# Kernel tuning notes

Hardware: AMD Instinct MI355X
Metric: run time of the kernel (lower is better)

The kernel has to match this reference:

```python
import jax, jax.numpy as jnp
import numpy as np

DROPOUT_P = 0.0  # undefined global `dropout_p` in source; pinned to 0 (identity) for determinism


def setup_inputs() -> dict:
    key = jax.random.key(0)
    k1, k2, k3 = jax.random.split(key, 3)
    B, Lq, Lk, D = 16, 4096, 4096, 64
    return {
        "query": jax.random.normal(k1, (B, Lq, D), dtype=jnp.float32),
        "key": jax.random.normal(k2, (B, Lk, D), dtype=jnp.float32),
        "value": jax.random.normal(k3, (B, Lk, D), dtype=jnp.float32),
        "scale_factor": jnp.ones((1,), dtype=jnp.float32),
    }


def reference(query, key, value, scale_factor):
    # scores: [B, Lq, Lk] -- the large HBM-materialized intermediate
    scores = jnp.einsum("bqd,bkd->bqk", query, key) / scale_factor
    probs = jax.nn.softmax(scores, axis=-1)
    # dropout with p = DROPOUT_P = 0.0 is the identity
    out = jnp.einsum("bqk,bkd->bqd", probs, value)
    return out
```

## Files before the change

kernel.cpp:

```cpp
#include <hip/hip_runtime.h>
#include <hip/hip_fp16.h>

typedef _Float16 half2_t __attribute__((ext_vector_type(2)));
typedef _Float16 half4_t __attribute__((ext_vector_type(4)));
typedef _Float16 half8_t __attribute__((ext_vector_type(8)));
typedef float   float4_t __attribute__((ext_vector_type(4)));
typedef float  float16_t __attribute__((ext_vector_type(16)));

static __device__ __forceinline__ half2_t cvt_pk(float a, float b) {
    return __builtin_bit_cast(half2_t, __builtin_amdgcn_cvt_pkrtz(a, b));
}
static __device__ __forceinline__ half4_t cvt_pk4(float a, float b, float c, float d) {
    half2_t lo = cvt_pk(a, b), hi = cvt_pk(c, d);
    half4_t r;
    r[0] = lo[0]; r[1] = lo[1]; r[2] = hi[0]; r[3] = hi[1];
    return r;
}
static __device__ __forceinline__ half8_t cvt_pk8(const float4& a, const float4& b) {
    half4_t lo = cvt_pk4(a.x, a.y, a.z, a.w);
    half4_t hi = cvt_pk4(b.x, b.y, b.z, b.w);
    return __builtin_shufflevector(lo, hi, 0, 1, 2, 3, 4, 5, 6, 7);
}
static __device__ __forceinline__ half8_t join8(half4_t lo, half4_t hi) {
    return __builtin_shufflevector(lo, hi, 0, 1, 2, 3, 4, 5, 6, 7);
}

namespace {
constexpr int kB       = 16;
constexpr int kL       = 4096;
constexpr int kD       = 64;
constexpr int kQTile   = 128;
constexpr int kBK      = 64;
constexpr int kTiles   = kL / kBK;
constexpr int kSplit   = 2;
constexpr int kTilesHf = kTiles / kSplit;
constexpr int kTileH   = kBK * kD;
constexpr int kKStride = 72;
constexpr int kVStride = 72;
constexpr size_t kWsHalves = (size_t)kB * kTiles * kTileH;
constexpr size_t kOHalves  = (size_t)kB * kL * kD;
}


__global__ __launch_bounds__(256) void prep_kv(const float* __restrict__ K,
                                               const float* __restrict__ V,
                                               _Float16* __restrict__ Kws,
                                               _Float16* __restrict__ Vws)
{
    int blk = blockIdx.x;
    const int tid = threadIdx.x;
    if (blk < kB * kTiles) {
        const float* src = K + (size_t)blk * kTileH;
        _Float16* dst = Kws + (size_t)blk * kTileH;
#pragma unroll
        for (int i = 0; i < 2; ++i) {
            const int task = tid + 256 * i;
            const int row  = task >> 3;
            const int g    = task & 7;
            const int srow = (row & ~12) | ((row & 4) << 1) | ((row & 8) >> 1);
            const float* p = src + srow * kD + g * 8;
            const float4 a  = *(const float4*)p;
            const float4 b2 = *(const float4*)(p + 4);
            *(half8_t*)(dst + task * 8) = cvt_pk8(a, b2);
        }
    } else {
        blk -= kB * kTiles;
        const float* src = V + (size_t)blk * kTileH;
        _Float16* dst = Vws + (size_t)blk * kTileH;
        const int d  = tid & 63;
        const int vw = tid >> 6;
#pragma unroll
        for (int i = 0; i < 2; ++i) {
            const int c8 = vw * 2 + i;
            const int k0 = c8 * 8;
            float p[8];
#pragma unroll
            for (int j = 0; j < 8; ++j) p[j] = src[(k0 + j) * kD + d];
            half4_t lo = cvt_pk4(p[0], p[1], p[2], p[3]);
            half4_t hi = cvt_pk4(p[4], p[5], p[6], p[7]);
            *(half8_t*)(dst + (c8 * 64 + d) * 8) = join8(lo, hi);
        }
    }
}

__global__ __launch_bounds__(256, 3)
void fa_fwd(const float* __restrict__ Q, const _Float16* __restrict__ Kws,
            const _Float16* __restrict__ Vws, const float* __restrict__ scale_ptr,
            float* __restrict__ Out, _Float16* __restrict__ O2ws,
            float* __restrict__ Mlws)
{
    __shared__ __align__(16) _Float16 Ksh[kBK * kKStride];
    __shared__ __align__(16) _Float16 Vsh[kD * kVStride];

    const int tid  = threadIdx.x;
    const int wave = tid >> 6;
    const int lane = tid & 63;
    const int l31  = lane & 31;
    const int hi   = lane >> 5;

    const int b  = blockIdx.y;
    const int hf = blockIdx.z;
    const int q0 = blockIdx.x * kQTile + wave * 32;

    const int task0 = tid, task1 = tid + 256;
    const int vd = tid & 63;
    const int vw = tid >> 6;

    const float qscale = 1.4426950408889634f / scale_ptr[0];

    const float*    Qb = Q   + (size_t)b * kL * kD;
    const _Float16* Kt = Kws + ((size_t)b * kTiles + (size_t)hf * kTilesHf) * kTileH;
    const _Float16* Vt = Vws + ((size_t)b * kTiles + (size_t)hf * kTilesHf) * kTileH;

    half8_t qfrag[4];
    {
        const float* qrow = Qb + (size_t)(q0 + l31) * kD;
#pragma unroll
        for (int kd = 0; kd < 4; ++kd) {
            const float* p = qrow + kd * 16 + hi * 8;
            half8_t h;
#pragma unroll
            for (int j = 0; j < 8; ++j) h[j] = (_Float16)(p[j] * qscale);
            qfrag[kd] = h;
        }
    }

    float16_t O[2];
    O[0] = (float16_t)0.0f;
    O[1] = (float16_t)0.0f;
    float m_run = -__builtin_inff();
    float l_run = 0.0f;
    const float16_t Zc = (float16_t)0.0f;

    half8_t kp[2], vp[2];
    kp[0] = *(const half8_t*)(Kt + task0 * 8);
    kp[1] = *(const half8_t*)(Kt + task1 * 8);
    vp[0] = *(const half8_t*)(Vt + ((vw * 2 + 0) * 64 + vd) * 8);
    vp[1] = *(const half8_t*)(Vt + ((vw * 2 + 1) * 64 + vd) * 8);

    for (int t = 0; t < kTilesHf; ++t) {
        __syncthreads();

        *(half8_t*)(&Ksh[(task0 >> 3) * kKStride + (task0 & 7) * 8]) = kp[0];
        *(half8_t*)(&Ksh[(task1 >> 3) * kKStride + (task1 & 7) * 8]) = kp[1];
        *(half8_t*)(&Vsh[vd * kVStride + (vw * 2 + 0) * 8]) = vp[0];
        *(half8_t*)(&Vsh[vd * kVStride + (vw * 2 + 1) * 8]) = vp[1];
        __syncthreads();

        {
            const int nt = (t + 1) & (kTilesHf - 1);
            const _Float16* kn = Kt + (size_t)nt * kTileH;
            const _Float16* vn = Vt + (size_t)nt * kTileH;
            kp[0] = *(const half8_t*)(kn + task0 * 8);
            kp[1] = *(const half8_t*)(kn + task1 * 8);
            vp[0] = *(const half8_t*)(vn + ((vw * 2 + 0) * 64 + vd) * 8);
            vp[1] = *(const half8_t*)(vn + ((vw * 2 + 1) * 64 + vd) * 8);
        }

        float16_t S0, S1;
        {
            half8_t kf0, kf1;
            kf0 = *(const half8_t*)(&Ksh[(l31)      * kKStride + 0 * 16 + hi * 8]);
            kf1 = *(const half8_t*)(&Ksh[(32 + l31) * kKStride + 0 * 16 + hi * 8]);
            S0 = __builtin_amdgcn_mfma_f32_32x32x16_f16(kf0, qfrag[0], Zc, 0, 0, 0);
            S1 = __builtin_amdgcn_mfma_f32_32x32x16_f16(kf1, qfrag[0], Zc, 0, 0, 0);
#pragma unroll
            for (int kd = 1; kd < 4; ++kd) {
                kf0 = *(const half8_t*)(&Ksh[(l31)      * kKStride + kd * 16 + hi * 8]);
                kf1 = *(const half8_t*)(&Ksh[(32 + l31) * kKStride + kd * 16 + hi * 8]);
                S0 = __builtin_amdgcn_mfma_f32_32x32x16_f16(kf0, qfrag[kd], S0, 0, 0, 0);
                S1 = __builtin_amdgcn_mfma_f32_32x32x16_f16(kf1, qfrag[kd], S1, 0, 0, 0);
            }
        }

#define M4(v,a) fmaxf(fmaxf(v[a], v[(a)+1]), fmaxf(v[(a)+2], v[(a)+3]))
        float pm = fmaxf(
            fmaxf(fmaxf(M4(S0, 0), M4(S0, 4)), fmaxf(M4(S0, 8), M4(S0, 12))),
            fmaxf(fmaxf(M4(S1, 0), M4(S1, 4)), fmaxf(M4(S1, 8), M4(S1, 12))));
#undef M4
        pm = fmaxf(pm, __shfl_xor(pm, 32));

        const bool need = pm > m_run + 8.0f;
        if (__ballot(need)) {
            const float mn    = fmaxf(m_run, pm);
            const float alpha = __builtin_amdgcn_exp2f(m_run - mn);
            m_run = mn;
            l_run *= alpha;
#pragma unroll
            for (int r = 0; r < 16; ++r) { O[0][r] *= alpha; O[1][r] *= alpha; }
        }

#pragma unroll
        for (int r = 0; r < 16; ++r) {
            S0[r] = __builtin_amdgcn_exp2f(S0[r] - m_run);
            S1[r] = __builtin_amdgcn_exp2f(S1[r] - m_run);
        }
        half8_t pf[4];
        pf[0] = join8(cvt_pk4(S0[0],  S0[1],  S0[2],  S0[3]),
                      cvt_pk4(S0[4],  S0[5],  S0[6],  S0[7]));
        pf[1] = join8(cvt_pk4(S0[8],  S0[9],  S0[10], S0[11]),
                      cvt_pk4(S0[12], S0[13], S0[14], S0[15]));
        pf[2] = join8(cvt_pk4(S1[0],  S1[1],  S1[2],  S1[3]),
                      cvt_pk4(S1[4],  S1[5],  S1[6],  S1[7]));
        pf[3] = join8(cvt_pk4(S1[8],  S1[9],  S1[10], S1[11]),
                      cvt_pk4(S1[12], S1[13], S1[14], S1[15]));
#define A4(v,a) ((v[a] + v[(a)+1]) + (v[(a)+2] + v[(a)+3]))
        float lt = ((A4(S0, 0) + A4(S0, 4)) + (A4(S0, 8) + A4(S0, 12)))
                 + ((A4(S1, 0) + A4(S1, 4)) + (A4(S1, 8) + A4(S1, 12)));
#undef A4
        lt += __shfl_xor(lt, 32);
        l_run += lt;

#pragma unroll
        for (int kb = 0; kb < 4; ++kb) {
            const half8_t vf0 = *(const half8_t*)(
                &Vsh[(l31)      * kVStride + kb * 16 + hi * 8]);
            const half8_t vf1 = *(const half8_t*)(
                &Vsh[(32 + l31) * kVStride + kb * 16 + hi * 8]);
            O[0] = __builtin_amdgcn_mfma_f32_32x32x16_f16(vf0, pf[kb], O[0], 0, 0, 0);
            O[1] = __builtin_amdgcn_mfma_f32_32x32x16_f16(vf1, pf[kb], O[1], 0, 0, 0);
        }
    }

    const float inv = 1.0f / l_run;
    const int   q   = q0 + l31;
    if (hf == 0) {
        float* op = Out + ((size_t)b * kL + q) * kD;
#pragma unroll
        for (int dt = 0; dt < 2; ++dt)
#pragma unroll
            for (int rr = 0; rr < 4; ++rr) {
                const int d0 = dt * 32 + rr * 8 + hi * 4;
                float4 w;
                w.x = O[dt][rr * 4 + 0] * inv;
                w.y = O[dt][rr * 4 + 1] * inv;
                w.z = O[dt][rr * 4 + 2] * inv;
                w.w = O[dt][rr * 4 + 3] * inv;
                *(float4*)(op + d0) = w;
            }
    } else {
        _Float16* op = O2ws + ((size_t)b * kL + q) * kD;
#pragma unroll
        for (int dt = 0; dt < 2; ++dt)
#pragma unroll
            for (int rr = 0; rr < 4; ++rr) {
                const int d0 = dt * 32 + rr * 8 + hi * 4;
                half4_t w = cvt_pk4(O[dt][rr * 4 + 0] * inv, O[dt][rr * 4 + 1] * inv,
                                    O[dt][rr * 4 + 2] * inv, O[dt][rr * 4 + 3] * inv);
                *(half4_t*)(op + d0) = w;
            }
    }
    if (hi == 0) {
        float* mp = Mlws + (((size_t)b * kL + q) * 2 + hf) * 2;
        mp[0] = m_run;
        mp[1] = l_run;
    }
}

__global__ __launch_bounds__(256)
void combine(float* __restrict__ Out, const _Float16* __restrict__ O2ws,
             const float* __restrict__ Mlws)
{
    const int t   = threadIdx.x;
    const int row = blockIdx.x * 16 + (t >> 4);
    const int d0  = (t & 15) * 4;

    const float m1 = Mlws[(size_t)row * 4 + 0];
    const float l1 = Mlws[(size_t)row * 4 + 1];
    const float m2 = Mlws[(size_t)row * 4 + 2];
    const float l2 = Mlws[(size_t)row * 4 + 3];

    const float m  = fmaxf(m1, m2);
    float w1 = l1 * exp2f(m1 - m);
    float w2 = l2 * exp2f(m2 - m);
    const float inv = 1.0f / (w1 + w2);
    w1 *= inv; w2 *= inv;

    float* op = Out + (size_t)row * kD + d0;
    const _Float16* o2 = O2ws + (size_t)row * kD + d0;
    float4 a = *(const float4*)op;
    const half4_t h = *(const half4_t*)o2;
    a.x = a.x * w1 + (float)h[0] * w2;
    a.y = a.y * w1 + (float)h[1] * w2;
    a.z = a.z * w1 + (float)h[2] * w2;
    a.w = a.w * w1 + (float)h[3] * w2;
    *(float4*)op = a;
}

extern "C" void kernel_launch(void* const* d_in, const int* in_sizes, int n_in,
                              void* d_out, int out_size, void* d_ws, size_t ws_size,
                              hipStream_t stream) {
    const float* Q = (const float*)d_in[0];
    const float* K = (const float*)d_in[1];
    const float* V = (const float*)d_in[2];
    const float* s = (const float*)d_in[3];
    float* out = (float*)d_out;
    _Float16* Kws  = (_Float16*)d_ws;
    _Float16* Vws  = Kws + kWsHalves;
    _Float16* O2ws = Vws + kWsHalves;
    float*    Mlws = (float*)(O2ws + kOHalves);

    prep_kv<<<dim3(2 * kB * kTiles), dim3(256), 0, stream>>>(K, V, Kws, Vws);
    fa_fwd<<<dim3(kL / kQTile, kB, kSplit), dim3(256), 0, stream>>>(Q, Kws, Vws, s, out, O2ws, Mlws);
    combine<<<dim3(kB * kL / 16), dim3(256), 0, stream>>>(out, O2ws, Mlws);
}
```

Baseline: 188.5 us.

## Double-buffer K/V shared tiles, add MFMA priority hints, defer row-sum shuffle

K and V tiles are double-buffered in LDS, so each iteration writes the next tile into the alternate buffer and only one barrier per iteration is needed instead of two. Global prefetch now runs two tiles ahead. The change also raises the occupancy hint to 4 blocks per CU, wraps the MFMA sections in s_setprio, rebuilds the max reduction with 3-input fmax (max3), and moves the cross-half row-sum shuffle out of the loop to the epilogue. The costs are twice the LDS use and a tighter register budget, which may cause spills.

```diff
diff --git a/kernel.cpp b/kernel.cpp
--- a/kernel.cpp
+++ b/kernel.cpp
@@ -23,6 +23,9 @@
 }
 static __device__ __forceinline__ half8_t join8(half4_t lo, half4_t hi) {
     return __builtin_shufflevector(lo, hi, 0, 1, 2, 3, 4, 5, 6, 7);
+}
+static __device__ __forceinline__ float f3(float a, float b, float c) {
+    return fmaxf(fmaxf(a, b), c);
 }
 
 namespace {
@@ -83,14 +86,14 @@
     }
 }
 
-__global__ __launch_bounds__(256, 3)
+__global__ __launch_bounds__(256, 4)
 void fa_fwd(const float* __restrict__ Q, const _Float16* __restrict__ Kws,
             const _Float16* __restrict__ Vws, const float* __restrict__ scale_ptr,
             float* __restrict__ Out, _Float16* __restrict__ O2ws,
             float* __restrict__ Mlws)
 {
-    __shared__ __align__(16) _Float16 Ksh[kBK * kKStride];
-    __shared__ __align__(16) _Float16 Vsh[kD * kVStride];
+    __shared__ __align__(16) _Float16 Ksh[2][kBK * kKStride];
+    __shared__ __align__(16) _Float16 Vsh[2][kD * kVStride];
 
     const int tid  = threadIdx.x;
     const int wave = tid >> 6;
@@ -105,6 +108,10 @@
     const int task0 = tid, task1 = tid + 256;
     const int vd = tid & 63;
     const int vw = tid >> 6;
+    const int koff0 = (task0 >> 3) * kKStride + (task0 & 7) * 8;
+    const int koff1 = (task1 >> 3) * kKStride + (task1 & 7) * 8;
+    const int voff0 = vd * kVStride + (vw * 2 + 0) * 8;
+    const int voff1 = vd * kVStride + (vw * 2 + 1) * 8;
 
     const float qscale = 1.4426950408889634f / scale_ptr[0];
 
@@ -137,18 +144,34 @@
     kp[1] = *(const half8_t*)(Kt + task1 * 8);
     vp[0] = *(const half8_t*)(Vt + ((vw * 2 + 0) * 64 + vd) * 8);
     vp[1] = *(const half8_t*)(Vt + ((vw * 2 + 1) * 64 + vd) * 8);
+    *(half8_t*)(&Ksh[0][koff0]) = kp[0];
+    *(half8_t*)(&Ksh[0][koff1]) = kp[1];
+    *(half8_t*)(&Vsh[0][voff0]) = vp[0];
+    *(half8_t*)(&Vsh[0][voff1]) = vp[1];
+    {
+        const _Float16* kn = Kt + (size_t)1 * kTileH;
+        const _Float16* vn = Vt + (size_t)1 * kTileH;
+        kp[0] = *(const half8_t*)(kn + task0 * 8);
+        kp[1] = *(const half8_t*)(kn + task1 * 8);
+        vp[0] = *(const half8_t*)(vn + ((vw * 2 + 0) * 64 + vd) * 8);
+        vp[1] = *(const half8_t*)(vn + ((vw * 2 + 1) * 64 + vd) * 8);
+    }
+    __syncthreads();
 
     for (int t = 0; t < kTilesHf; ++t) {
-        __syncthreads();
-
-        *(half8_t*)(&Ksh[(task0 >> 3) * kKStride + (task0 & 7) * 8]) = kp[0];
-        *(half8_t*)(&Ksh[(task1 >> 3) * kKStride + (task1 & 7) * 8]) = kp[1];
-        *(half8_t*)(&Vsh[vd * kVStride + (vw * 2 + 0) * 8]) = vp[0];
-        *(half8_t*)(&Vsh[vd * kVStride + (vw * 2 + 1) * 8]) = vp[1];
-        __syncthreads();
+        const int cur = t & 1;
+        const _Float16* Kb = Ksh[cur];
+        const _Float16* Vb = Vsh[cur];
+        _Float16* Kn = Ksh[cur ^ 1];
+        _Float16* Vn = Vsh[cur ^ 1];
+
+        *(half8_t*)(&Kn[koff0]) = kp[0];
+        *(half8_t*)(&Kn[koff1]) = kp[1];
+        *(half8_t*)(&Vn[voff0]) = vp[0];
+        *(half8_t*)(&Vn[voff1]) = vp[1];
 
         {
-            const int nt = (t + 1) & (kTilesHf - 1);
+            const int nt = (t + 2) & (kTilesHf - 1);
             const _Float16* kn = Kt + (size_t)nt * kTileH;
             const _Float16* vn = Vt + (size_t)nt * kTileH;
             kp[0] = *(const half8_t*)(kn + task0 * 8);
@@ -160,24 +183,36 @@
         float16_t S0, S1;
         {
             half8_t kf0, kf1;
-            kf0 = *(const half8_t*)(&Ksh[(l31)      * kKStride + 0 * 16 + hi * 8]);
-            kf1 = *(const half8_t*)(&Ksh[(32 + l31) * kKStride + 0 * 16 + hi * 8]);
+            kf0 = *(const half8_t*)(&Kb[(l31)      * kKStride + 0 * 16 + hi * 8]);
+            kf1 = *(const half8_t*)(&Kb[(32 + l31) * kKStride + 0 * 16 + hi * 8]);
+            __builtin_amdgcn_s_setprio(1);
             S0 = __builtin_amdgcn_mfma_f32_32x32x16_f16(kf0, qfrag[0], Zc, 0, 0, 0);
             S1 = __builtin_amdgcn_mfma_f32_32x32x16_f16(kf1, qfrag[0], Zc, 0, 0, 0);
 #pragma unroll
             for (int kd = 1; kd < 4; ++kd) {
-                kf0 = *(const half8_t*)(&Ksh[(l31)      * kKStride + kd * 16 + hi * 8]);
-                kf1 = *(const half8_t*)(&Ksh[(32 + l31) * kKStride + kd * 16 + hi * 8]);
+                kf0 = *(const half8_t*)(&Kb[(l31)      * kKStride + kd * 16 + hi * 8]);
+                kf1 = *(const half8_t*)(&Kb[(32 + l31) * kKStride + kd * 16 + hi * 8]);
                 S0 = __builtin_amdgcn_mfma_f32_32x32x16_f16(kf0, qfrag[kd], S0, 0, 0, 0);
                 S1 = __builtin_amdgcn_mfma_f32_32x32x16_f16(kf1, qfrag[kd], S1, 0, 0, 0);
             }
-        }
-
-#define M4(v,a) fmaxf(fmaxf(v[a], v[(a)+1]), fmaxf(v[(a)+2], v[(a)+3]))
-        float pm = fmaxf(
-            fmaxf(fmaxf(M4(S0, 0), M4(S0, 4)), fmaxf(M4(S0, 8), M4(S0, 12))),
-            fmaxf(fmaxf(M4(S1, 0), M4(S1, 4)), fmaxf(M4(S1, 8), M4(S1, 12))));
-#undef M4
+            __builtin_amdgcn_s_setprio(0);
+        }
+
+        float v0 = f3(S0[0],  S0[1],  S0[2]);
+        float v1 = f3(S0[3],  S0[4],  S0[5]);
+        float v2 = f3(S0[6],  S0[7],  S0[8]);
+        float v3 = f3(S0[9],  S0[10], S0[11]);
+        float v4 = f3(S0[12], S0[13], S0[14]);
+        float v5 = f3(S0[15], S1[0],  S1[1]);
+        float v6 = f3(S1[2],  S1[3],  S1[4]);
+        float v7 = f3(S1[5],  S1[6],  S1[7]);
+        float v8 = f3(S1[8],  S1[9],  S1[10]);
+        float v9 = f3(S1[11], S1[12], S1[13]);
+        float w0 = f3(v0, v1, v2);
+        float w1 = f3(v3, v4, v5);
+        float w2 = f3(v6, v7, v8);
+        float w3 = f3(v9, S1[14], S1[15]);
+        float pm = fmaxf(fmaxf(w0, w1), fmaxf(w2, w3));
         pm = fmaxf(pm, __shfl_xor(pm, 32));
 
         const bool need = pm > m_run + 8.0f;
@@ -205,23 +240,26 @@
         pf[3] = join8(cvt_pk4(S1[8],  S1[9],  S1[10], S1[11]),
                       cvt_pk4(S1[12], S1[13], S1[14], S1[15]));
 #define A4(v,a) ((v[a] + v[(a)+1]) + (v[(a)+2] + v[(a)+3]))
-        float lt = ((A4(S0, 0) + A4(S0, 4)) + (A4(S0, 8) + A4(S0, 12)))
-                 + ((A4(S1, 0) + A4(S1, 4)) + (A4(S1, 8) + A4(S1, 12)));
+        l_run += ((A4(S0, 0) + A4(S0, 4)) + (A4(S0, 8) + A4(S0, 12)))
+               + ((A4(S1, 0) + A4(S1, 4)) + (A4(S1, 8) + A4(S1, 12)));
 #undef A4
-        lt += __shfl_xor(lt, 32);
-        l_run += lt;
-
+
+        __builtin_amdgcn_s_setprio(1);
 #pragma unroll
         for (int kb = 0; kb < 4; ++kb) {
             const half8_t vf0 = *(const half8_t*)(
-                &Vsh[(l31)      * kVStride + kb * 16 + hi * 8]);
+                &Vb[(l31)      * kVStride + kb * 16 + hi * 8]);
             const half8_t vf1 = *(const half8_t*)(
-                &Vsh[(32 + l31) * kVStride + kb * 16 + hi * 8]);
+                &Vb[(32 + l31) * kVStride + kb * 16 + hi * 8]);
             O[0] = __builtin_amdgcn_mfma_f32_32x32x16_f16(vf0, pf[kb], O[0], 0, 0, 0);
             O[1] = __builtin_amdgcn_mfma_f32_32x32x16_f16(vf1, pf[kb], O[1], 0, 0, 0);
         }
-    }
-
+        __builtin_amdgcn_s_setprio(0);
+
+        __syncthreads();
+    }
+
+    l_run += __shfl_xor(l_run, 32);
     const float inv = 1.0f / l_run;
     const int   q   = q0 + l31;
     if (hf == 0) {
@@ -251,9 +289,8 @@
             }
     }
     if (hi == 0) {
-        float* mp = Mlws + (((size_t)b * kL + q) * 2 + hf) * 2;
-        mp[0] = m_run;
-        mp[1] = l_run;
+        float2 ml; ml.x = m_run; ml.y = l_run;
+        *(float2*)(Mlws + (((size_t)b * kL + q) * 2 + hf) * 2) = ml;
     }
 }
 
```

After: 186.0 us. No clear change (-1.3%).
